# Performance work log

Hardware: AMD Instinct MI355X
Metric: run time of the kernel (lower is better)

The kernel has to match this reference:

```python
import jax, jax.numpy as jnp
import numpy as np

B, C, H, W = 16, 192, 56, 56   # feature map from visual encoder
K = 9                          # kNN neighbors (knn_graph k)
NUM_CLASSES = 100
PRED_DIM = 1024                # pred_emb_dim
EPS = 1e-5                     # BatchNorm eps


def setup_inputs() -> dict:
    key = jax.random.key(0)
    ks = jax.random.split(key, 6)
    def kaiming(k, shape, fan_in):
        return jax.random.normal(k, shape, jnp.float32) * np.float32(np.sqrt(2.0 / fan_in))
    return {
        "image_feature_map": jax.random.normal(ks[0], (B, C, H, W), jnp.float32),
        # 1x1 conv patch-prediction head: Conv2d(C, NUM_CLASSES, 1)
        "conv_w": kaiming(ks[1], (NUM_CLASSES, C), C),
        "conv_b": jnp.zeros((NUM_CLASSES,), jnp.float32),
        # stand-in for opaque GSAT GNN: one linear + mean neighbor aggregation
        "gnn_w": kaiming(ks[2], (C, C), C),
        "gnn_b": jnp.zeros((C,), jnp.float32),
        # prediction head: Linear(C, PRED_DIM) -> BN -> GELU -> Linear(PRED_DIM, NUM_CLASSES)
        "w1": kaiming(ks[3], (C, PRED_DIM), C),
        "b1": jnp.zeros((PRED_DIM,), jnp.float32),
        "bn_gamma": jnp.ones((PRED_DIM,), jnp.float32),
        "bn_beta": jnp.zeros((PRED_DIM,), jnp.float32),
        "w2": kaiming(ks[4], (PRED_DIM, NUM_CLASSES), PRED_DIM),
        "b2": jnp.zeros((NUM_CLASSES,), jnp.float32),
    }


def _knn_edges(x_norm):
    """x_norm: [B, N, C] L2-normalized. Per-image kNN (no cross-batch edges,
    no self loops). Returns global (src, dst) of shape [B*N*K] each,
    src = neighbor, dst = center node (PyG source_to_target flow)."""
    N = x_norm.shape[1]
    # normalized vectors: argmin Euclidean dist == argmax cosine sim
    sim = jnp.einsum('bnc,bmc->bnm', x_norm, x_norm)          # [B,N,N]
    sim = sim - 4.0 * jnp.eye(N, dtype=sim.dtype)             # exclude self
    _, nbr = jax.lax.top_k(sim, K)                            # [B,N,K]
    offs = (jnp.arange(B) * N)[:, None, None]
    src = (nbr + offs).reshape(-1)
    dst = (jnp.broadcast_to(jnp.arange(N)[None, :, None], (B, N, K)) + offs).reshape(-1)
    return src, dst


def reference(image_feature_map, conv_w, conv_b, gnn_w, gnn_b,
              w1, b1, bn_gamma, bn_beta, w2, b2):
    N = H * W
    # patch predictions: 1x1 conv over feature map
    patch_pred = jnp.einsum('bchw,kc->bkhw', image_feature_map, conv_w) + conv_b[None, :, None, None]
    # reshape_into_graph_input: [B,C,H,W] -> [B*N, C] nodes, then L2 normalize
    x = image_feature_map.reshape(B, C, N).transpose(0, 2, 1)  # [B,N,C]
    x = x / jnp.maximum(jnp.linalg.norm(x, axis=-1, keepdims=True), 1e-12)
    # knn_graph under no_grad
    src, dst = _knn_edges(jax.lax.stop_gradient(x))
    nodes = x.reshape(B * N, C)
    # GNN stand-in: linear + relu, edge attention, mean neighbor aggregation
    h = jax.nn.relu(nodes @ gnn_w + gnn_b)                     # [B*N, C]
    raw_edge_att = jnp.sum(h[src] * h[dst], axis=-1)           # [B*N*K]
    edge_att = jax.nn.sigmoid(raw_edge_att)
    msg = jax.ops.segment_sum(h[src], dst, num_segments=B * N)
    h = h + msg / np.float32(K)
    # global_add_pool over batch assignment
    batch = jnp.repeat(jnp.arange(B), N)
    g = jax.ops.segment_sum(h, batch, num_segments=B)          # [B, C]
    # prediction MLP: Linear -> BatchNorm1d (train-mode batch stats) -> GELU -> Linear
    z = g @ w1 + b1
    mu = jnp.mean(z, axis=0)
    var = jnp.var(z, axis=0)
    z = (z - mu) * jax.lax.rsqrt(var + EPS) * bn_gamma + bn_beta
    z = jax.nn.gelu(z, approximate=False)
    pred = z @ w2 + b2                                         # [B, NUM_CLASSES]
    return (pred, edge_att, patch_pred)
```

## Files before the change

### kernel.cpp

```cpp
#include <hip/hip_runtime.h>
#include <math.h>

#define B_  16
#define C_  192
#define N_  3136
#define BN_ 50176
#define K_  9
#define NC_ 100
#define PD_ 1024
#define NSEV 7
#define SEVCOLS 448

#define OUT_EATT 1600
#define OUT_PP   453184

typedef short bf16x8 __attribute__((ext_vector_type(8)));
typedef float f32x16 __attribute__((ext_vector_type(16)));

__device__ __forceinline__ unsigned int umaxu(unsigned int a, unsigned int b) { return a > b ? a : b; }
__device__ __forceinline__ unsigned int med3u(unsigned int a, unsigned int b, unsigned int c) {
    unsigned int d;
    asm("v_med3_u32 %0, %1, %2, %3" : "=v"(d) : "v"(a), "v"(b), "v"(c));
    return d;
}
__device__ __forceinline__ void ins12m(unsigned int (&lk)[12], unsigned int key) {
    unsigned int nk[12];
    nk[0] = umaxu(lk[0], key);
    #pragma unroll
    for (int k = 1; k < 12; ++k) nk[k] = med3u(lk[k - 1], lk[k], key);
    #pragma unroll
    for (int k = 0; k < 12; ++k) lk[k] = nk[k];
}

template<int NL>
__device__ inline void ins_lex(float (&lv)[NL], int (&li)[NL], float v, int vi) {
    if (v > lv[NL-1] || (v == lv[NL-1] && vi < li[NL-1])) {
        #pragma unroll
        for (int k = 0; k < NL; ++k) {
            bool p = (v > lv[k]) || (v == lv[k] && vi < li[k]);
            float fv = p ? lv[k] : v; int fi = p ? li[k] : vi;
            lv[k] = p ? v : lv[k];    li[k] = p ? vi : li[k];
            v = fv; vi = fi;
        }
    }
}

__device__ inline unsigned int bf16_rne(unsigned int u) {
    return (u + 0x7fffu + ((u >> 16) & 1u)) & 0xffff0000u;
}

__global__ __launch_bounds__(256) void k_normalize(const float* __restrict__ in,
        float* __restrict__ xn, unsigned short* __restrict__ xsn,
        float* __restrict__ norms) {
    __shared__ float tile[C_][65];
    __shared__ float part[4][64];
    __shared__ float rnorm_s[64];
    int b = blockIdx.x & 15;
    int n0 = (blockIdx.x >> 4) * 64;
    int t = threadIdx.x;
    for (int f = t; f < C_ * 64; f += 256) {
        int c = f >> 6, n = f & 63;
        tile[c][n] = in[((size_t)b * C_ + c) * N_ + n0 + n];
    }
    __syncthreads();
    {
        int n = t & 63, qq = t >> 6;
        float s = 0.f;
        #pragma unroll
        for (int i = 0; i < 48; ++i) { float v = tile[qq * 48 + i][n]; s += v * v; }
        part[qq][n] = s;
    }
    __syncthreads();
    if (t < 64) {
        float tot = part[0][t] + part[1][t] + part[2][t] + part[3][t];
        float nrm = fmaxf(sqrtf(tot), 1e-12f);
        norms[(size_t)b * N_ + n0 + t] = nrm;
        rnorm_s[t] = 1.0f / nrm;
    }
    __syncthreads();
    for (int f = t; f < 64 * 96; f += 256) {
        int n = f / 96, cp = f - n * 96;
        int c = cp * 2;
        float r = rnorm_s[n];
        float v0 = tile[c][n] * r;
        float v1 = tile[c + 1][n] * r;
        size_t row = (size_t)b * N_ + n0 + n;
        *(float2*)(xn + row * C_ + c) = make_float2(v0, v1);
        unsigned int h0 = bf16_rne(__float_as_uint(v0));
        unsigned int h1 = bf16_rne(__float_as_uint(v1));
        unsigned int l0 = bf16_rne(__float_as_uint(v0 - __uint_as_float(h0)));
        unsigned int l1 = bf16_rne(__float_as_uint(v1 - __uint_as_float(h1)));
        unsigned int* xr = (unsigned int*)(xsn + row * 384);
        xr[cp]      = (h0 >> 16) | (h1 & 0xffff0000u);
        xr[96 + cp] = (l0 >> 16) | (l1 & 0xffff0000u);
    }
}

__global__ __launch_bounds__(256) void k_wsplit(const float* __restrict__ cw,
        const float* __restrict__ gw, const float* __restrict__ w2,
        unsigned short* __restrict__ wsc, unsigned short* __restrict__ wsg,
        float* __restrict__ w2t) {
    int id = blockIdx.x * 256 + threadIdx.x;
    if (id < 128 * 192) {
        int k = id / 192, c = id - k * 192;
        float v = (k < 100) ? cw[k * 192 + c] : 0.f;
        unsigned int h = bf16_rne(__float_as_uint(v));
        wsc[(size_t)k * 384 + c] = (unsigned short)(h >> 16);
        wsc[(size_t)k * 384 + 192 + c] =
            (unsigned short)(bf16_rne(__float_as_uint(v - __uint_as_float(h))) >> 16);
    } else if (id < 61440) {
        int e = id - 128 * 192;
        int cc = e / 192, j = e - cc * 192;
        float v = gw[cc * 192 + j];
        unsigned int h = bf16_rne(__float_as_uint(v));
        wsg[(size_t)j * 384 + cc] = (unsigned short)(h >> 16);
        wsg[(size_t)j * 384 + 192 + cc] =
            (unsigned short)(bf16_rne(__float_as_uint(v - __uint_as_float(h))) >> 16);
    } else {
        int e2 = id - 61440;
        int jj = e2 >> 10, k = e2 & 1023;
        w2t[(size_t)jj * PD_ + k] = w2[(size_t)k * NC_ + jj];
    }
}

#define STAGE32(DST, SRCBASE, NLW) { \
    const char* s_ = (SRCBASE); \
    _Pragma("unroll") \
    for (int q_ = 0; q_ < NLW; ++q_) \
        __builtin_amdgcn_global_load_lds( \
            (const __attribute__((address_space(1))) unsigned int*)(s_ + q_ * 32), \
            (__attribute__((address_space(3))) unsigned int*)((DST) + (w * NLW + q_) * 1024), 16, 0, 0); }

#define STAGEHALF(DST, BASE, COLB, KH, NLW) { \
    _Pragma("unroll") \
    for (int q_ = 0; q_ < NLW; ++q_) { \
        const char* s_ = (BASE) + (size_t)((COLB) + l31) * 768 + (KH) * 384 + (w * (NLW) + q_) * 32 + lh * 16; \
        __builtin_amdgcn_global_load_lds( \
            (const __attribute__((address_space(1))) unsigned int*)s_, \
            (__attribute__((address_space(3))) unsigned int*)((DST) + (w * (NLW) + q_) * 1024), 16, 0, 0); } }

#define SCAN16 { \
    int c0 = cbase + c * 32 + 4 * lh; \
    int selfslot = r - c0; \
    int kc = 4095 - c0; \
    _Pragma("unroll") \
    for (int g = 0; g < 4; ++g) { \
        _Pragma("unroll") \
        for (int q = 0; q < 4; ++q) { \
            unsigned int u = __float_as_uint(fmaf(acc[4 * g + q], 0.125f, 0.75f)); \
            unsigned int key = ((u >> 3) << 12) | (unsigned int)(kc - (8 * g + q)); \
            key = (8 * g + q == selfslot) ? 0u : key; \
            ins12m(lk, key); \
        } \
    } }

__global__ __launch_bounds__(256, 3) void k_simmfma(const unsigned short* __restrict__ xs,
        unsigned int* __restrict__ topk) {
    __shared__ __align__(1024) char SMEM[24576];
    int bid = blockIdx.x;
    int img = bid & 15;
    int rest = bid >> 4;
    int rb = rest / NSEV;
    int sv = rest - rb * NSEV;
    int t = threadIdx.x;
    int w = t >> 6, lane = t & 63;
    int l31 = lane & 31, lh = lane >> 5;
    const char* xsi = (const char*)(xs + (size_t)img * N_ * 384);

    int r = rb * 128 + w * 32 + l31;
    bool valid = r < N_;
    int rl = valid ? r : (N_ - 1);
    bf16x8 bfrag[24];
    {
        const char* rp = xsi + (size_t)rl * 768 + lh * 16;
        #pragma unroll
        for (int ks = 0; ks < 24; ++ks)
            bfrag[ks] = *(const bf16x8*)(rp + ks * 32);
    }
    unsigned int lk[12];
    #pragma unroll
    for (int k = 0; k < 12; ++k) lk[k] = 0u;

    int cbase = sv * SEVCOLS;

    STAGEHALF(SMEM, xsi, cbase, 0, 3)
    __syncthreads();

    for (int c = 0; c < 14; ++c) {
        STAGEHALF(SMEM + 12288, xsi, cbase + c * 32, 1, 3)
        f32x16 acc;
        #pragma unroll
        for (int i = 0; i < 16; ++i) acc[i] = 0.f;
        {
            const char* rp = SMEM + lh * 512 + l31 * 16;
            __builtin_amdgcn_s_setprio(1);
            #pragma unroll
            for (int ks = 0; ks < 12; ++ks) {
                bf16x8 af = *(const bf16x8*)(rp + ks * 1024);
                acc = __builtin_amdgcn_mfma_f32_32x32x16_bf16(af, bfrag[ks], acc, 0, 0, 0);
            }
            __builtin_amdgcn_s_setprio(0);
        }
        __syncthreads();
        if (c < 13) { STAGEHALF(SMEM, xsi, cbase + (c + 1) * 32, 0, 3) }
        {
            const char* rp = SMEM + 12288 + lh * 512 + l31 * 16;
            __builtin_amdgcn_s_setprio(1);
            #pragma unroll
            for (int ks = 0; ks < 12; ++ks) {
                bf16x8 af = *(const bf16x8*)(rp + ks * 1024);
                acc = __builtin_amdgcn_mfma_f32_32x32x16_bf16(af, bfrag[12 + ks], acc, 0, 0, 0);
            }
            __builtin_amdgcn_s_setprio(0);
        }
        if (valid) SCAN16
        __syncthreads();
    }
    unsigned int pk[12];
    #pragma unroll
    for (int j = 0; j < 12; ++j)
        pk[j] = (unsigned int)__shfl_xor((int)lk[j], 32, 64);
    #pragma unroll
    for (int j = 0; j < 12; ++j) ins12m(lk, pk[j]);
    if (valid && lh == 0) {
        unsigned int* op = topk + ((size_t)sv * BN_ + (size_t)img * N_ + r) * 12;
        #pragma unroll
        for (int k = 0; k < 12; ++k) op[k] = lk[k];
    }
}

__global__ __launch_bounds__(256, 3) void k_patchmfma(const unsigned short* __restrict__ xs,
        const unsigned short* __restrict__ wsc, const float* __restrict__ norms,
        const float* __restrict__ cb, float* __restrict__ outp) {
    __shared__ __align__(1024) char SMEM[24576];
    int bid = blockIdx.x;
    int img = bid & 15;
    int n0 = (bid >> 4) * 64;
    int t = threadIdx.x;
    int w = t >> 6, lane = t & 63;
    int l31 = lane & 31, lh = lane >> 5;
    const char* xsi = (const char*)(xs + (size_t)img * N_ * 384);
    int ch = w * 32 + l31;
    bf16x8 bfrag[24];
    {
        const char* wp = (const char*)wsc + (size_t)ch * 768 + lh * 16;
        #pragma unroll
        for (int ks = 0; ks < 24; ++ks)
            bfrag[ks] = *(const bf16x8*)(wp + ks * 32);
    }
    float bias = (ch < NC_) ? cb[ch] : 0.f;
    STAGEHALF(SMEM, xsi, n0, 0, 3)
    __syncthreads();
    for (int c = 0; c < 2; ++c) {
        STAGEHALF(SMEM + 12288, xsi, n0 + c * 32, 1, 3)
        f32x16 acc;
        #pragma unroll
        for (int i = 0; i < 16; ++i) acc[i] = 0.f;
        {
            const char* rp = SMEM + lh * 512 + l31 * 16;
            #pragma unroll
            for (int ks = 0; ks < 12; ++ks) {
                bf16x8 af = *(const bf16x8*)(rp + ks * 1024);
                acc = __builtin_amdgcn_mfma_f32_32x32x16_bf16(af, bfrag[ks], acc, 0, 0, 0);
            }
        }
        __syncthreads();
        if (c == 0) { STAGEHALF(SMEM, xsi, n0 + 32, 0, 3) }
        {
            const char* rp = SMEM + 12288 + lh * 512 + l31 * 16;
            #pragma unroll
            for (int ks = 0; ks < 12; ++ks) {
                bf16x8 af = *(const bf16x8*)(rp + ks * 1024);
                acc = __builtin_amdgcn_mfma_f32_32x32x16_bf16(af, bfrag[12 + ks], acc, 0, 0, 0);
            }
        }
        if (ch < NC_) {
            int nb = n0 + c * 32 + 4 * lh;
            float* op = outp + ((size_t)(img * NC_ + ch)) * N_ + nb;
            const float* npv = norms + (size_t)img * N_ + nb;
            #pragma unroll
            for (int g = 0; g < 4; ++g) {
                float4 nv = *(const float4*)(npv + 8 * g);
                float4 o;
                o.x = acc[4 * g + 0] * nv.x + bias;
                o.y = acc[4 * g + 1] * nv.y + bias;
                o.z = acc[4 * g + 2] * nv.z + bias;
                o.w = acc[4 * g + 3] * nv.w + bias;
                *(float4*)(op + 8 * g) = o;
            }
        }
        __syncthreads();
    }
}

__global__ __launch_bounds__(384, 3) void k_gnnmfma(const unsigned short* __restrict__ xs,
        const unsigned short* __restrict__ wsg, const float* __restrict__ gbias,
        float* __restrict__ h) {
    __shared__ __align__(1024) char SMEM[49152];
    int n0 = blockIdx.x * 128;
    int t = threadIdx.x;
    int w = t / 64, lane = t & 63;
    int l31 = lane & 31, lh = lane >> 5;
    int j = w * 32 + l31;
    bf16x8 bfrag[24];
    {
        const char* wp = (const char*)wsg + (size_t)j * 768 + lh * 16;
        #pragma unroll
        for (int ks = 0; ks < 24; ++ks)
            bfrag[ks] = *(const bf16x8*)(wp + ks * 32);
    }
    float bj = gbias[j];
    STAGE32(SMEM, (const char*)xs + (size_t)(n0 + l31) * 768 + w * 128 + lh * 16, 4);
    __syncthreads();
    for (int c = 0; c < 4; ++c) {
        char* cur = SMEM + (c & 1) * 24576;
        if (c < 3) {
            char* dst = SMEM + ((c & 1) ^ 1) * 24576;
            STAGE32(dst, (const char*)xs + (size_t)(n0 + (c + 1) * 32 + l31) * 768 + w * 128 + lh * 16, 4);
        }
        f32x16 acc;
        #pragma unroll
        for (int i = 0; i < 16; ++i) acc[i] = 0.f;
        const char* rp = cur + lh * 512 + l31 * 16;
        #pragma unroll
        for (int ks = 0; ks < 24; ++ks) {
            bf16x8 af = *(const bf16x8*)(rp + ks * 1024);
            acc = __builtin_amdgcn_mfma_f32_32x32x16_bf16(af, bfrag[ks], acc, 0, 0, 0);
        }
        int nb = n0 + c * 32 + 4 * lh;
        #pragma unroll
        for (int g = 0; g < 4; ++g)
            #pragma unroll
            for (int q = 0; q < 4; ++q)
                h[(size_t)(nb + 8 * g + q) * C_ + j] = fmaxf(acc[4 * g + q] + bj, 0.f);
        __syncthreads();
    }
}

__global__ __launch_bounds__(256) void k_merge2(const unsigned int* __restrict__ topk,
        int* __restrict__ nbr12) {
    int row = blockIdx.x * 256 + threadIdx.x;
    unsigned int lk[12];
    const unsigned int* p0 = topk + (size_t)row * 12;
    #pragma unroll
    for (int k = 0; k < 12; ++k) lk[k] = p0[k];
    #pragma unroll
    for (int h = 1; h < NSEV; ++h) {
        const unsigned int* p1 = topk + ((size_t)h * BN_ + row) * 12;
        #pragma unroll
        for (int j = 0; j < 12; ++j) ins12m(lk, p1[j]);
    }
    int gb = (row / N_) * N_;
    int* np = nbr12 + (size_t)row * 12;
    #pragma unroll
    for (int k = 0; k < 12; ++k) np[k] = gb + (4095 - (int)(lk[k] & 0xFFFu));
}

__global__ __launch_bounds__(256) void k_rescore(const float* __restrict__ xn,
        const int* __restrict__ nbr12, int* __restrict__ nbr9) {
    int img = blockIdx.x & 15;
    int sub = blockIdx.x >> 4;
    int t = threadIdx.x;
    int lane = t & 63;
    int row = img * N_ + sub * 16 + (t >> 4);
    int c = lane & 15;
    int cand = nbr12[(size_t)row * 12 + (c < 12 ? c : 0)];
    const float4* xa = (const float4*)(xn + (size_t)row * C_);
    const float4* xb = (const float4*)(xn + (size_t)cand * C_);
    float dot = 0.f;
    #pragma unroll
    for (int k = 0; k < 48; ++k) {
        float4 p = xa[k], q = xb[k];
        dot += p.x*q.x + p.y*q.y + p.z*q.z + p.w*q.w;
    }
    float v = (c < 12 && cand != row) ? dot : -1e30f;
    float lv[9]; int li[9];
    #pragma unroll
    for (int k = 0; k < 9; ++k) { lv[k] = -1e30f; li[k] = 0x7fffffff; }
    int gbase = lane & 48;
    #pragma unroll
    for (int j = 0; j < 12; ++j) {
        float vj = __shfl(v, gbase + j, 64);
        int  ij = __shfl(cand, gbase + j, 64);
        ins_lex<9>(lv, li, vj, ij);
    }
    if (c == 0) {
        int* np = nbr9 + (size_t)row * 9;
        #pragma unroll
        for (int k = 0; k < 9; ++k) np[k] = li[k];
    }
}

__global__ __launch_bounds__(256) void k_edge(const float* __restrict__ h,
        const int* __restrict__ nbr, float* __restrict__ eatt,
        float* __restrict__ gparte) {
    __shared__ float ps[4][C_];
    int img = blockIdx.x & 15;
    int sub = blockIdx.x >> 4;
    int t = threadIdx.x;
    int wv = t >> 6;
    int nl = t >> 4;
    int l16 = t & 15;
    int node = img * N_ + sub * 16 + nl;
    const float4* hc = (const float4*)(h + (size_t)node * C_) + l16;
    float4 c0 = hc[0], c1 = hc[16], c2 = hc[32];
    float4 m0 = make_float4(0,0,0,0), m1 = make_float4(0,0,0,0), m2 = make_float4(0,0,0,0);
    const int* np_ = nbr + (size_t)node * K_;
    float* ep = eatt + (size_t)node * K_;
    #pragma unroll
    for (int k = 0; k < K_; ++k) {
        int src = np_[k];
        const float4* hs = (const float4*)(h + (size_t)src * C_) + l16;
        float4 s0 = hs[0], s1 = hs[16], s2 = hs[32];
        float d = s0.x*c0.x + s0.y*c0.y + s0.z*c0.z + s0.w*c0.w
                + s1.x*c1.x + s1.y*c1.y + s1.z*c1.z + s1.w*c1.w
                + s2.x*c2.x + s2.y*c2.y + s2.z*c2.z + s2.w*c2.w;
        d += __shfl_xor(d, 1, 64);
        d += __shfl_xor(d, 2, 64);
        d += __shfl_xor(d, 4, 64);
        d += __shfl_xor(d, 8, 64);
        if (l16 == 0) ep[k] = 1.0f / (1.0f + expf(-d));
        m0.x += s0.x; m0.y += s0.y; m0.z += s0.z; m0.w += s0.w;
        m1.x += s1.x; m1.y += s1.y; m1.z += s1.z; m1.w += s1.w;
        m2.x += s2.x; m2.y += s2.y; m2.z += s2.z; m2.w += s2.w;
    }
    const float r9 = 1.0f / 9.0f;
    float v[12];
    v[0] = c0.x + m0.x * r9; v[1]  = c0.y + m0.y * r9;
    v[2] = c0.z + m0.z * r9; v[3]  = c0.w + m0.w * r9;
    v[4] = c1.x + m1.x * r9; v[5]  = c1.y + m1.y * r9;
    v[6] = c1.z + m1.z * r9; v[7]  = c1.w + m1.w * r9;
    v[8] = c2.x + m2.x * r9; v[9]  = c2.y + m2.y * r9;
    v[10] = c2.z + m2.z * r9; v[11] = c2.w + m2.w * r9;
    #pragma unroll
    for (int e = 0; e < 12; ++e) {
        v[e] += __shfl_xor(v[e], 16, 64);
        v[e] += __shfl_xor(v[e], 32, 64);
    }
    if ((t & 63) < 16) {
        #pragma unroll
        for (int j = 0; j < 3; ++j)
            #pragma unroll
            for (int e = 0; e < 4; ++e)
                ps[wv][j * 64 + l16 * 4 + e] = v[j * 4 + e];
    }
    __syncthreads();
    if (t < C_)
        gparte[(size_t)blockIdx.x * C_ + t] =
            (ps[0][t] + ps[1][t]) + (ps[2][t] + ps[3][t]);
}

__global__ __launch_bounds__(192) void k_gred(const float* __restrict__ gparte,
        float* __restrict__ gpart) {
    int b = blockIdx.x >> 2, s = blockIdx.x & 3;
    int oc = threadIdx.x;
    float acc = 0.f;
    for (int sub = s * 49; sub < (s + 1) * 49; ++sub)
        acc += gparte[((size_t)(sub * 16 + b)) * C_ + oc];
    gpart[(size_t)(b * 4 + s) * C_ + oc] = acc;
}

__global__ __launch_bounds__(256) void k_mlp1(const float* __restrict__ gpart,
        const float* __restrict__ w1, const float* __restrict__ b1,
        const float* __restrict__ gam, const float* __restrict__ bet,
        float* __restrict__ zs) {
    __shared__ float gs[B_ * C_];
    int t = threadIdx.x;
    int j = blockIdx.x * 256 + t;
    for (int f = t; f < B_ * C_; f += 256) {
        int b = f / C_, oc = f - b * C_;
        float a = 0.f;
        #pragma unroll
        for (int s = 0; s < 4; ++s) a += gpart[((size_t)(b * 4 + s)) * C_ + oc];
        gs[f] = a;
    }
    __syncthreads();
    float z[16];
    #pragma unroll
    for (int i = 0; i < 16; ++i) z[i] = b1[j];
    for (int c = 0; c < C_; ++c) {
        float w = w1[(size_t)c * PD_ + j];
        #pragma unroll
        for (int i = 0; i < 16; ++i) z[i] += gs[i * C_ + c] * w;
    }
    float mu = 0.f;
    #pragma unroll
    for (int i = 0; i < 16; ++i) mu += z[i];
    mu *= (1.0f / 16.0f);
    float var = 0.f;
    #pragma unroll
    for (int i = 0; i < 16; ++i) { float d = z[i] - mu; var += d * d; }
    var *= (1.0f / 16.0f);
    float sc = (1.0f / sqrtf(var + 1e-5f)) * gam[j];
    float bt = bet[j];
    #pragma unroll
    for (int i = 0; i < 16; ++i) {
        float zh = (z[i] - mu) * sc + bt;
        zs[(size_t)i * PD_ + j] = 0.5f * zh * (1.0f + erff(zh * 0.70710678118654752f));
    }
}

__global__ __launch_bounds__(64) void k_mlp2(const float* __restrict__ zs,
        const float* __restrict__ w2t, const float* __restrict__ b2,
        float* __restrict__ pred) {
    int i = blockIdx.x / NC_, jj = blockIdx.x - i * NC_;
    int lane = threadIdx.x;
    const float* zr = zs + (size_t)i * PD_;
    const float* wr = w2t + (size_t)jj * PD_;
    float a = 0.f;
    #pragma unroll
    for (int k = 0; k < 16; ++k) a += zr[lane + 64 * k] * wr[lane + 64 * k];
    a += __shfl_xor(a, 1, 64);  a += __shfl_xor(a, 2, 64);
    a += __shfl_xor(a, 4, 64);  a += __shfl_xor(a, 8, 64);
    a += __shfl_xor(a, 16, 64); a += __shfl_xor(a, 32, 64);
    if (lane == 0) pred[i * NC_ + jj] = a + b2[jj];
}

extern "C" void kernel_launch(void* const* d_in, const int* in_sizes, int n_in,
                              void* d_out, int out_size, void* d_ws, size_t ws_size,
                              hipStream_t stream) {
    const float* img    = (const float*)d_in[0];
    const float* conv_w = (const float*)d_in[1];
    const float* conv_b = (const float*)d_in[2];
    const float* gnn_w  = (const float*)d_in[3];
    const float* gnn_b  = (const float*)d_in[4];
    const float* w1     = (const float*)d_in[5];
    const float* b1     = (const float*)d_in[6];
    const float* bng    = (const float*)d_in[7];
    const float* bnb    = (const float*)d_in[8];
    const float* w2     = (const float*)d_in[9];
    const float* b2     = (const float*)d_in[10];
    float* out = (float*)d_out;

    float* XN            = (float*)d_ws;
    unsigned short* XS   = (unsigned short*)(XN + (size_t)BN_ * C_);
    unsigned int* TOPK   = (unsigned int*)(XS + (size_t)BN_ * 384);
    int*   NBR12         = (int*)(TOPK + (size_t)NSEV * BN_ * 12);
    int*   NBR9          = NBR12 + (size_t)BN_ * 12;
    float* NORMS         = (float*)(NBR9 + (size_t)BN_ * K_);
    unsigned short* WSC  = (unsigned short*)(NORMS + BN_);
    unsigned short* WSG  = WSC + (size_t)128 * 384;
    float* GPART         = (float*)(WSG + (size_t)192 * 384);
    float* W2T           = GPART + (size_t)128 * C_;
    float* Hh            = XN;
    float* GPARTE        = (float*)TOPK;
    float* ZS            = (float*)NBR12;

    k_normalize<<<784, 256, 0, stream>>>(img, XN, XS, NORMS);
    k_wsplit   <<<640, 256, 0, stream>>>(conv_w, gnn_w, w2, WSC, WSG, W2T);
    k_patchmfma<<<784, 256, 0, stream>>>(XS, WSC, NORMS, conv_b, out + OUT_PP);
    k_simmfma  <<<2800, 256, 0, stream>>>(XS, TOPK);
    k_merge2   <<<196, 256, 0, stream>>>(TOPK, NBR12);
    k_rescore  <<<3136, 256, 0, stream>>>(XN, NBR12, NBR9);
    k_gnnmfma  <<<392, 384, 0, stream>>>(XS, WSG, gnn_b, Hh);
    k_edge     <<<3136, 256, 0, stream>>>(Hh, NBR9, out + OUT_EATT, GPARTE);
    k_gred     <<<64, 192, 0, stream>>>(GPARTE, GPART);
    k_mlp1     <<<4, 256, 0, stream>>>(GPART, w1, b1, bng, bnb, ZS);
    k_mlp2     <<<1600, 64, 0, stream>>>(ZS, W2T, b2, out);
}
```

Baseline: 416.1 us.

## Raise occupancy bounds, skip self-mask outside diagonal tile, coalesce rescore dots

The kNN similarity kernel now applies the self-exclusion check only on the one column tile that contains the row's own index, and uses a cheaper scan everywhere else. The minimum-blocks hint in the launch bounds goes from 3 to 5 for the similarity kernel and from 3 to 4 for the patch kernel, which pushes the compiler toward fewer registers and higher occupancy. The rescore kernel changes from one thread per candidate reading a whole row serially to 16 lanes reading each row in a coalesced pattern and combining partial sums with a shuffle reduction. The tighter register budgets risk spilling in the MFMA kernels, which keep 24 bf16x8 fragments in registers.

```diff
diff --git a/kernel.cpp b/kernel.cpp
--- a/kernel.cpp
+++ b/kernel.cpp
@@ -141,6 +141,18 @@
 
 #define SCAN16 { \
     int c0 = cbase + c * 32 + 4 * lh; \
+    int kc = 4095 - c0; \
+    _Pragma("unroll") \
+    for (int g = 0; g < 4; ++g) { \
+        _Pragma("unroll") \
+        for (int q = 0; q < 4; ++q) { \
+            unsigned int u = __float_as_uint(fmaf(acc[4 * g + q], 0.125f, 0.75f)); \
+            unsigned int key = ((u >> 3) << 12) | (unsigned int)(kc - (8 * g + q)); \
+            ins12m(lk, key); \
+        } \
+    } }
+#define SCAN16D { \
+    int c0 = cbase + c * 32 + 4 * lh; \
     int selfslot = r - c0; \
     int kc = 4095 - c0; \
     _Pragma("unroll") \
@@ -154,7 +166,7 @@
         } \
     } }
 
-__global__ __launch_bounds__(256, 3) void k_simmfma(const unsigned short* __restrict__ xs,
+__global__ __launch_bounds__(256, 5) void k_simmfma(const unsigned short* __restrict__ xs,
         unsigned int* __restrict__ topk) {
     __shared__ __align__(1024) char SMEM[24576];
     int bid = blockIdx.x;
@@ -182,6 +194,7 @@
     for (int k = 0; k < 12; ++k) lk[k] = 0u;
 
     int cbase = sv * SEVCOLS;
+    int c_self = rb * 4 + w - sv * 14;
 
     STAGEHALF(SMEM, xsi, cbase, 0, 3)
     __syncthreads();
@@ -213,7 +226,10 @@
             }
             __builtin_amdgcn_s_setprio(0);
         }
-        if (valid) SCAN16
+        if (valid) {
+            if (c == c_self) SCAN16D
+            else             SCAN16
+        }
         __syncthreads();
     }
     unsigned int pk[12];
@@ -229,7 +245,7 @@
     }
 }
 
-__global__ __launch_bounds__(256, 3) void k_patchmfma(const unsigned short* __restrict__ xs,
+__global__ __launch_bounds__(256, 4) void k_patchmfma(const unsigned short* __restrict__ xs,
         const unsigned short* __restrict__ wsc, const float* __restrict__ norms,
         const float* __restrict__ cb, float* __restrict__ outp) {
     __shared__ __align__(1024) char SMEM[24576];
@@ -361,30 +377,33 @@
     int img = blockIdx.x & 15;
     int sub = blockIdx.x >> 4;
     int t = threadIdx.x;
-    int lane = t & 63;
-    int row = img * N_ + sub * 16 + (t >> 4);
-    int c = lane & 15;
-    int cand = nbr12[(size_t)row * 12 + (c < 12 ? c : 0)];
-    const float4* xa = (const float4*)(xn + (size_t)row * C_);
-    const float4* xb = (const float4*)(xn + (size_t)cand * C_);
-    float dot = 0.f;
-    #pragma unroll
-    for (int k = 0; k < 48; ++k) {
-        float4 p = xa[k], q = xb[k];
-        dot += p.x*q.x + p.y*q.y + p.z*q.z + p.w*q.w;
-    }
-    float v = (c < 12 && cand != row) ? dot : -1e30f;
+    int nl = t >> 4, l16 = t & 15;
+    int row = img * N_ + sub * 16 + nl;
+    const float4* xa = (const float4*)(xn + (size_t)row * C_) + l16;
+    float4 a0 = xa[0], a1 = xa[16], a2 = xa[32];
+    const int* np12 = nbr12 + (size_t)row * 12;
+    float d[12]; int ci[12];
+    #pragma unroll
+    for (int j = 0; j < 12; ++j) {
+        int cand = np12[j];
+        ci[j] = cand;
+        const float4* xb = (const float4*)(xn + (size_t)cand * C_) + l16;
+        float4 b0 = xb[0], b1 = xb[16], b2 = xb[32];
+        float s = a0.x*b0.x + a0.y*b0.y + a0.z*b0.z + a0.w*b0.w
+                + a1.x*b1.x + a1.y*b1.y + a1.z*b1.z + a1.w*b1.w
+                + a2.x*b2.x + a2.y*b2.y + a2.z*b2.z + a2.w*b2.w;
+        s += __shfl_xor(s, 1, 64);
+        s += __shfl_xor(s, 2, 64);
+        s += __shfl_xor(s, 4, 64);
+        s += __shfl_xor(s, 8, 64);
+        d[j] = (cand != row) ? s : -1e30f;
+    }
     float lv[9]; int li[9];
     #pragma unroll
     for (int k = 0; k < 9; ++k) { lv[k] = -1e30f; li[k] = 0x7fffffff; }
-    int gbase = lane & 48;
-    #pragma unroll
-    for (int j = 0; j < 12; ++j) {
-        float vj = __shfl(v, gbase + j, 64);
-        int  ij = __shfl(cand, gbase + j, 64);
-        ins_lex<9>(lv, li, vj, ij);
-    }
-    if (c == 0) {
+    #pragma unroll
+    for (int j = 0; j < 12; ++j) ins_lex<9>(lv, li, d[j], ci[j]);
+    if (l16 == 0) {
         int* np = nbr9 + (size_t)row * 9;
         #pragma unroll
         for (int k = 0; k < 9; ++k) np[k] = li[k];
```

Result: slower. 657.6 us (+58.1%).
